# Performance work log

Hardware: AMD Instinct MI355X
Metric: run time of the kernel (lower is better)

## Reference

```python
import jax, jax.numpy as jnp
import numpy as np

N_NODES = 100000
N_EDGES = 1600000
F_IN = 128
F_OUT = 64


def setup_inputs() -> dict:
    key = jax.random.key(0)
    k0, k1, k2, k3, k4, k5 = jax.random.split(key, 6)
    stdv = 1.0 / np.sqrt(F_OUT)
    x = jax.random.normal(k0, (N_NODES, F_IN), dtype=jnp.float32)
    edge_src = jax.random.randint(k1, (N_EDGES,), 0, N_NODES, dtype=jnp.int32)
    edge_dst = jax.random.randint(k2, (N_EDGES,), 0, N_NODES, dtype=jnp.int32)
    # normalized adjacency values (all positive, like D^-1/2 A D^-1/2 entries)
    edge_weight = jax.random.uniform(k3, (N_EDGES,), dtype=jnp.float32)
    weight = jax.random.uniform(k4, (F_IN, F_OUT), dtype=jnp.float32, minval=-stdv, maxval=stdv)
    bias = jax.random.uniform(k5, (F_OUT,), dtype=jnp.float32, minval=-stdv, maxval=stdv)
    return {"x": x, "edge_weight": edge_weight, "weight": weight, "bias": bias,
            "edge_src": edge_src, "edge_dst": edge_dst}


def reference(x, edge_weight, weight, bias, edge_src, edge_dst):
    # support = X @ W  -- dense GEMM [N, F_in] x [F_in, F_out]
    support = x @ weight
    # spmm(adj, support): adj in COO form; gather source rows, scale by edge value,
    # scatter-add into destination rows.
    msgs = support[edge_src] * edge_weight[:, None]          # [E, F_out]
    out = jax.ops.segment_sum(msgs, edge_dst, num_segments=x.shape[0])
    return out + bias
```

## Files before the change

kernel.cpp:

```cpp
#include <hip/hip_runtime.h>
#include <hip/hip_bf16.h>

#define F_IN 128
#define F_OUT 64
#define BUCKET_SHIFT 7
#define BUCKET_NODES 128
#define BUCKET_CAP 2880
#define CNT_STRIDE 16
#define NB_MAX 800
#define SCAT_CHUNK 16384
#define P1_GEMM_ROWS 64
#define LDK 136

typedef __attribute__((ext_vector_type(8))) short bf16x8;
typedef __attribute__((ext_vector_type(4))) float f32x4;

__device__ inline short bf16_bits(float f) {
  __hip_bfloat16 h = __float2bfloat16(f);
  return *reinterpret_cast<short*>(&h);
}

union Phase1Smem {
  struct { short As[P1_GEMM_ROWS][LDK]; short Bs[F_OUT][LDK]; } g;
  struct { int lhist[NB_MAX]; int lcur[NB_MAX]; } s;
};

__global__ __launch_bounds__(512, 8) void gcn_phase1_kernel(
    const float* __restrict__ x, const float* __restrict__ w,
    __hip_bfloat16* __restrict__ support,
    const int* __restrict__ esrc, const int* __restrict__ edst,
    const float* __restrict__ ew, int* __restrict__ bcount,
    int2* __restrict__ region, int n_nodes, int n_edges, int nb,
    int n_scat_blocks) {
  __shared__ Phase1Smem sm;
  const int tid = threadIdx.x;

  if ((int)blockIdx.x < n_scat_blocks) {
    const int e0 = blockIdx.x * SCAT_CHUNK;
    const int e1 = min(e0 + SCAT_CHUNK, n_edges);
    const int n_local = e1 - e0;

    for (int i = tid; i < nb; i += 512) sm.s.lhist[i] = 0;
    __syncthreads();
    for (int i = tid; i < n_local; i += 512) {
      atomicAdd(&sm.s.lhist[edst[e0 + i] >> BUCKET_SHIFT], 1);
    }
    __syncthreads();
    for (int b = tid; b < nb; b += 512) {
      const int c = sm.s.lhist[b];
      sm.s.lcur[b] = c ? atomicAdd(&bcount[b * CNT_STRIDE], c) : 0;
    }
    __syncthreads();
    for (int i = tid; i < n_local; i += 512) {
      const int d = edst[e0 + i];
      const int b = d >> BUCKET_SHIFT;
      const int pos = atomicAdd(&sm.s.lcur[b], 1);
      if (pos < BUCKET_CAP) {
        region[(size_t)b * BUCKET_CAP + pos] =
            make_int2((esrc[e0 + i] << BUCKET_SHIFT) | (d & (BUCKET_NODES - 1)),
                      __float_as_int(ew[e0 + i]));
      }
    }
  } else {
    const int gbid = (int)blockIdx.x - n_scat_blocks;
    const int block_row = gbid * P1_GEMM_ROWS;

#pragma unroll
    for (int i = 0; i < F_IN * F_OUT / 512; ++i) {
      const int idx = tid + i * 512;
      sm.g.Bs[idx & 63][idx >> 6] = bf16_bits(w[idx]);
    }
#pragma unroll
    for (int i = 0; i < P1_GEMM_ROWS * (F_IN / 4) / 512; ++i) {
      const int idx = tid + i * 512;
      const int row = idx >> 5;
      const int c4 = idx & 31;
      float4 v = make_float4(0.f, 0.f, 0.f, 0.f);
      if (block_row + row < n_nodes)
        v = ((const float4*)(x + (size_t)(block_row + row) * F_IN))[c4];
      short4 b;
      b.x = bf16_bits(v.x);
      b.y = bf16_bits(v.y);
      b.z = bf16_bits(v.z);
      b.w = bf16_bits(v.w);
      *(short4*)&sm.g.As[row][c4 * 4] = b;
    }
    __syncthreads();

    const int lane = tid & 63;
    const int wid = tid >> 6;
    const int wr0 = (wid >> 1) * 16;
    const int wc0 = (wid & 1) * 32;
    const int m = lane & 15;
    const int quad = lane >> 4;

    f32x4 acc0 = {0.f, 0.f, 0.f, 0.f};
    f32x4 acc1 = {0.f, 0.f, 0.f, 0.f};
#pragma unroll
    for (int ks = 0; ks < 4; ++ks) {
      const int ko = ks * 32 + quad * 8;
      const bf16x8 a  = *(const bf16x8*)&sm.g.As[wr0 + m][ko];
      const bf16x8 b0 = *(const bf16x8*)&sm.g.Bs[wc0 + m][ko];
      const bf16x8 b1 = *(const bf16x8*)&sm.g.Bs[wc0 + 16 + m][ko];
      acc0 = __builtin_amdgcn_mfma_f32_16x16x32_bf16(a, b0, acc0, 0, 0, 0);
      acc1 = __builtin_amdgcn_mfma_f32_16x16x32_bf16(a, b1, acc1, 0, 0, 0);
    }
#pragma unroll
    for (int r = 0; r < 4; ++r) {
      const int row = block_row + wr0 + quad * 4 + r;
      if (row < n_nodes) {
        __hip_bfloat16* op = support + (size_t)row * F_OUT;
        op[wc0 + m]      = __float2bfloat16(acc0[r]);
        op[wc0 + 16 + m] = __float2bfloat16(acc1[r]);
      }
    }
  }
}

__global__ __launch_bounds__(512, 8) void gcn_sort_agg_kernel(
    const __hip_bfloat16* __restrict__ support,
    const int2* __restrict__ region, const int* __restrict__ bcount,
    const float* __restrict__ bias, float* __restrict__ out, int n_nodes) {
  __shared__ int2 outb[BUCKET_CAP];
  __shared__ int hist[BUCKET_NODES];
  __shared__ int nbeg[BUCKET_NODES];
  __shared__ int lcur[BUCKET_NODES];
  const int b = blockIdx.x;
  const int tid = threadIdx.x;
  const int lane = tid & 63;

  int cnt = bcount[b * CNT_STRIDE];
  cnt = (cnt < BUCKET_CAP ? cnt : BUCKET_CAP);
  const int2* reg = region + (size_t)b * BUCKET_CAP;

  for (int i = tid; i < BUCKET_NODES; i += 512) hist[i] = 0;
  __syncthreads();
  for (int i = tid; i < cnt; i += 512) {
    atomicAdd(&hist[reg[i].x & (BUCKET_NODES - 1)], 1);
  }
  __syncthreads();
  if (tid < 64) {
    const int v0 = hist[lane];
    const int v1 = hist[64 + lane];
    int s0 = v0;
#pragma unroll
    for (int off = 1; off < 64; off <<= 1) {
      const int t = __shfl_up(s0, off, 64);
      if (lane >= off) s0 += t;
    }
    const int tot0 = __shfl(s0, 63, 64);
    int s1 = v1;
#pragma unroll
    for (int off = 1; off < 64; off <<= 1) {
      const int t = __shfl_up(s1, off, 64);
      if (lane >= off) s1 += t;
    }
    s1 += tot0;
    nbeg[lane] = s0 - v0;
    nbeg[64 + lane] = s1 - v1;
    lcur[lane] = s0 - v0;
    lcur[64 + lane] = s1 - v1;
  }
  __syncthreads();
  for (int i = tid; i < cnt; i += 512) {
    const int2 p = reg[i];
    const int pos = atomicAdd(&lcur[p.x & (BUCKET_NODES - 1)], 1);
    outb[pos] = make_int2(p.x >> BUCKET_SHIFT, p.y);
  }
  __syncthreads();

  const int wid = tid >> 6;
  const int r = lane >> 4;
  const int c4 = (lane & 15) * 4;
  const ushort* sup = (const ushort*)support;
  const float4 b4 = *(const float4*)(bias + c4);
  for (int nl = wid * 16; nl < wid * 16 + 16; ++nl) {
    const int g = (b << BUCKET_SHIFT) + nl;
    if (g >= n_nodes) break;
    const int s = nbeg[nl];
    const int e = lcur[nl];
    f32x4 acc = {0.f, 0.f, 0.f, 0.f};
    for (int j = s; j < e; j += 4) {
      const int jr = j + r;
      const bool valid = jr < e;
      const int2 meta = outb[valid ? jr : e - 1];
      const float wv = valid ? __int_as_float(meta.y) : 0.f;
      const uint2 d = *(const uint2*)(sup + (size_t)meta.x * F_OUT + c4);
      acc[0] = fmaf(__uint_as_float(d.x << 16), wv, acc[0]);
      acc[1] = fmaf(__uint_as_float(d.x & 0xffff0000u), wv, acc[1]);
      acc[2] = fmaf(__uint_as_float(d.y << 16), wv, acc[2]);
      acc[3] = fmaf(__uint_as_float(d.y & 0xffff0000u), wv, acc[3]);
    }
#pragma unroll
    for (int i = 0; i < 4; ++i) {
      float v = acc[i];
      v += __shfl_xor(v, 16, 64);
      v += __shfl_xor(v, 32, 64);
      acc[i] = v;
    }
    if (r == 0) {
      float4 o;
      o.x = acc[0] + b4.x;
      o.y = acc[1] + b4.y;
      o.z = acc[2] + b4.z;
      o.w = acc[3] + b4.w;
      *(float4*)(out + (size_t)g * F_OUT + c4) = o;
    }
  }
}

extern "C" void kernel_launch(void* const* d_in, const int* in_sizes, int n_in,
                              void* d_out, int out_size, void* d_ws, size_t ws_size,
                              hipStream_t stream) {
  const float* x    = (const float*)d_in[0];
  const float* ew   = (const float*)d_in[1];
  const float* w    = (const float*)d_in[2];
  const float* bias = (const float*)d_in[3];
  const int*   esrc = (const int*)d_in[4];
  const int*   edst = (const int*)d_in[5];
  float* out = (float*)d_out;

  const int n_nodes = in_sizes[0] / F_IN;
  const int n_edges = in_sizes[4];
  const int nb = (n_nodes + BUCKET_NODES - 1) >> BUCKET_SHIFT;

  char* ws = (char*)d_ws;
  size_t off = 0;
  auto alloc = [&](size_t bytes) {
    size_t o = off;
    off += (bytes + 255) / 256 * 256;
    return o;
  };
  const size_t off_bcount  = alloc((size_t)nb * CNT_STRIDE * sizeof(int));
  const size_t off_region  = alloc((size_t)nb * BUCKET_CAP * sizeof(int2));
  const size_t off_support = alloc((size_t)n_nodes * F_OUT * sizeof(__hip_bfloat16));
  (void)off_support;

  int*  bcount = (int*)(ws + off_bcount);
  int2* region = (int2*)(ws + off_region);
  __hip_bfloat16* support = (__hip_bfloat16*)(ws + off_support);

  const int scat_blocks = (n_edges + SCAT_CHUNK - 1) / SCAT_CHUNK;
  const int gemm_blocks = (n_nodes + P1_GEMM_ROWS - 1) / P1_GEMM_ROWS;

  hipMemsetAsync(bcount, 0, (size_t)nb * CNT_STRIDE * sizeof(int), stream);
  gcn_phase1_kernel<<<scat_blocks + gemm_blocks, 512, 0, stream>>>(
      x, w, support, esrc, edst, ew, bcount, region, n_nodes, n_edges, nb,
      scat_blocks);
  gcn_sort_agg_kernel<<<nb, 512, 0, stream>>>(support, region, bcount, bias,
                                              out, n_nodes);
}
```

Baseline: 197.3 us.

## Cache edge dsts in LDS, load GEMM A directly to registers, unroll aggregation

```diff
diff --git a/kernel.cpp b/kernel.cpp
--- a/kernel.cpp
+++ b/kernel.cpp
@@ -8,7 +8,7 @@
 #define BUCKET_CAP 2880
 #define CNT_STRIDE 16
 #define NB_MAX 800
-#define SCAT_CHUNK 16384
+#define SCAT_CHUNK 8192
 #define P1_GEMM_ROWS 64
 #define LDK 136
 
@@ -21,11 +21,11 @@
 }
 
 union Phase1Smem {
-  struct { short As[P1_GEMM_ROWS][LDK]; short Bs[F_OUT][LDK]; } g;
-  struct { int lhist[NB_MAX]; int lcur[NB_MAX]; } s;
+  struct { short Bs[F_OUT][LDK]; } g;
+  struct { int lhist[NB_MAX]; int lcur[NB_MAX]; int ldst[SCAT_CHUNK]; } s;
 };
 
-__global__ __launch_bounds__(512, 8) void gcn_phase1_kernel(
+__global__ __launch_bounds__(512, 6) void gcn_phase1_kernel(
     const float* __restrict__ x, const float* __restrict__ w,
     __hip_bfloat16* __restrict__ support,
     const int* __restrict__ esrc, const int* __restrict__ edst,
@@ -43,7 +43,9 @@
     for (int i = tid; i < nb; i += 512) sm.s.lhist[i] = 0;
     __syncthreads();
     for (int i = tid; i < n_local; i += 512) {
-      atomicAdd(&sm.s.lhist[edst[e0 + i] >> BUCKET_SHIFT], 1);
+      const int d = edst[e0 + i];
+      sm.s.ldst[i] = d;
+      atomicAdd(&sm.s.lhist[d >> BUCKET_SHIFT], 1);
     }
     __syncthreads();
     for (int b = tid; b < nb; b += 512) {
@@ -52,7 +54,7 @@
     }
     __syncthreads();
     for (int i = tid; i < n_local; i += 512) {
-      const int d = edst[e0 + i];
+      const int d = sm.s.ldst[i];
       const int b = d >> BUCKET_SHIFT;
       const int pos = atomicAdd(&sm.s.lcur[b], 1);
       if (pos < BUCKET_CAP) {
@@ -70,22 +72,6 @@
       const int idx = tid + i * 512;
       sm.g.Bs[idx & 63][idx >> 6] = bf16_bits(w[idx]);
     }
-#pragma unroll
-    for (int i = 0; i < P1_GEMM_ROWS * (F_IN / 4) / 512; ++i) {
-      const int idx = tid + i * 512;
-      const int row = idx >> 5;
-      const int c4 = idx & 31;
-      float4 v = make_float4(0.f, 0.f, 0.f, 0.f);
-      if (block_row + row < n_nodes)
-        v = ((const float4*)(x + (size_t)(block_row + row) * F_IN))[c4];
-      short4 b;
-      b.x = bf16_bits(v.x);
-      b.y = bf16_bits(v.y);
-      b.z = bf16_bits(v.z);
-      b.w = bf16_bits(v.w);
-      *(short4*)&sm.g.As[row][c4 * 4] = b;
-    }
-    __syncthreads();
 
     const int lane = tid & 63;
     const int wid = tid >> 6;
@@ -93,23 +79,43 @@
     const int wc0 = (wid & 1) * 32;
     const int m = lane & 15;
     const int quad = lane >> 4;
+    const int row = block_row + wr0 + m;
+
+    bf16x8 afrag[4];
+    if (row < n_nodes) {
+      const float4* xr = (const float4*)(x + (size_t)row * F_IN);
+#pragma unroll
+      for (int ks = 0; ks < 4; ++ks) {
+        const float4 v0 = xr[ks * 8 + quad * 2];
+        const float4 v1 = xr[ks * 8 + quad * 2 + 1];
+        bf16x8 a;
+        a[0] = bf16_bits(v0.x); a[1] = bf16_bits(v0.y);
+        a[2] = bf16_bits(v0.z); a[3] = bf16_bits(v0.w);
+        a[4] = bf16_bits(v1.x); a[5] = bf16_bits(v1.y);
+        a[6] = bf16_bits(v1.z); a[7] = bf16_bits(v1.w);
+        afrag[ks] = a;
+      }
+    } else {
+#pragma unroll
+      for (int ks = 0; ks < 4; ++ks) afrag[ks] = (bf16x8)0;
+    }
+    __syncthreads();
 
     f32x4 acc0 = {0.f, 0.f, 0.f, 0.f};
     f32x4 acc1 = {0.f, 0.f, 0.f, 0.f};
 #pragma unroll
     for (int ks = 0; ks < 4; ++ks) {
       const int ko = ks * 32 + quad * 8;
-      const bf16x8 a  = *(const bf16x8*)&sm.g.As[wr0 + m][ko];
       const bf16x8 b0 = *(const bf16x8*)&sm.g.Bs[wc0 + m][ko];
       const bf16x8 b1 = *(const bf16x8*)&sm.g.Bs[wc0 + 16 + m][ko];
-      acc0 = __builtin_amdgcn_mfma_f32_16x16x32_bf16(a, b0, acc0, 0, 0, 0);
-      acc1 = __builtin_amdgcn_mfma_f32_16x16x32_bf16(a, b1, acc1, 0, 0, 0);
+      acc0 = __builtin_amdgcn_mfma_f32_16x16x32_bf16(afrag[ks], b0, acc0, 0, 0, 0);
+      acc1 = __builtin_amdgcn_mfma_f32_16x16x32_bf16(afrag[ks], b1, acc1, 0, 0, 0);
     }
 #pragma unroll
     for (int r = 0; r < 4; ++r) {
-      const int row = block_row + wr0 + quad * 4 + r;
-      if (row < n_nodes) {
-        __hip_bfloat16* op = support + (size_t)row * F_OUT;
+      const int orow = block_row + wr0 + quad * 4 + r;
+      if (orow < n_nodes) {
+        __hip_bfloat16* op = support + (size_t)orow * F_OUT;
         op[wc0 + m]      = __float2bfloat16(acc0[r]);
         op[wc0 + 16 + m] = __float2bfloat16(acc1[r]);
       }
@@ -117,7 +123,7 @@
   }
 }
 
-__global__ __launch_bounds__(512, 8) void gcn_sort_agg_kernel(
+__global__ __launch_bounds__(512, 6) void gcn_sort_agg_kernel(
     const __hip_bfloat16* __restrict__ support,
     const int2* __restrict__ region, const int* __restrict__ bcount,
     const float* __restrict__ bias, float* __restrict__ out, int n_nodes) {
@@ -179,31 +185,41 @@
     if (g >= n_nodes) break;
     const int s = nbeg[nl];
     const int e = lcur[nl];
-    f32x4 acc = {0.f, 0.f, 0.f, 0.f};
-    for (int j = s; j < e; j += 4) {
-      const int jr = j + r;
-      const bool valid = jr < e;
-      const int2 meta = outb[valid ? jr : e - 1];
-      const float wv = valid ? __int_as_float(meta.y) : 0.f;
-      const uint2 d = *(const uint2*)(sup + (size_t)meta.x * F_OUT + c4);
-      acc[0] = fmaf(__uint_as_float(d.x << 16), wv, acc[0]);
-      acc[1] = fmaf(__uint_as_float(d.x & 0xffff0000u), wv, acc[1]);
-      acc[2] = fmaf(__uint_as_float(d.y << 16), wv, acc[2]);
-      acc[3] = fmaf(__uint_as_float(d.y & 0xffff0000u), wv, acc[3]);
+    f32x4 acc0 = {0.f, 0.f, 0.f, 0.f};
+    f32x4 acc1 = {0.f, 0.f, 0.f, 0.f};
+    for (int j = s; j < e; j += 8) {
+      const int jr0 = j + r;
+      const int jr1 = j + 4 + r;
+      const bool va = jr0 < e;
+      const bool vb = jr1 < e;
+      const int2 m0 = outb[va ? jr0 : e - 1];
+      const int2 m1 = outb[vb ? jr1 : e - 1];
+      const float w0 = va ? __int_as_float(m0.y) : 0.f;
+      const float w1 = vb ? __int_as_float(m1.y) : 0.f;
+      const uint2 d0 = *(const uint2*)(sup + (size_t)m0.x * F_OUT + c4);
+      const uint2 d1 = *(const uint2*)(sup + (size_t)m1.x * F_OUT + c4);
+      acc0[0] = fmaf(__uint_as_float(d0.x << 16), w0, acc0[0]);
+      acc0[1] = fmaf(__uint_as_float(d0.x & 0xffff0000u), w0, acc0[1]);
+      acc0[2] = fmaf(__uint_as_float(d0.y << 16), w0, acc0[2]);
+      acc0[3] = fmaf(__uint_as_float(d0.y & 0xffff0000u), w0, acc0[3]);
+      acc1[0] = fmaf(__uint_as_float(d1.x << 16), w1, acc1[0]);
+      acc1[1] = fmaf(__uint_as_float(d1.x & 0xffff0000u), w1, acc1[1]);
+      acc1[2] = fmaf(__uint_as_float(d1.y << 16), w1, acc1[2]);
+      acc1[3] = fmaf(__uint_as_float(d1.y & 0xffff0000u), w1, acc1[3]);
     }
 #pragma unroll
     for (int i = 0; i < 4; ++i) {
-      float v = acc[i];
+      float v = acc0[i] + acc1[i];
       v += __shfl_xor(v, 16, 64);
       v += __shfl_xor(v, 32, 64);
-      acc[i] = v;
+      acc0[i] = v;
     }
     if (r == 0) {
       float4 o;
-      o.x = acc[0] + b4.x;
-      o.y = acc[1] + b4.y;
-      o.z = acc[2] + b4.z;
-      o.w = acc[3] + b4.w;
+      o.x = acc0[0] + b4.x;
+      o.y = acc0[1] + b4.y;
+      o.z = acc0[2] + b4.z;
+      o.w = acc0[3] + b4.w;
       *(float4*)(out + (size_t)g * F_OUT + c4) = o;
     }
   }
```

After: 181.4 us. 8.1% less time.
